# Performance work log

Hardware: AMD Instinct MI355X
Metric: run time of the kernel (lower is better)

Reference implementation:

```python
import jax, jax.numpy as jnp
import numpy as np

N, C_IN, C_OUT, H, W = 16, 256, 256, 32, 32
K = 9  # 3x3 kernel


def setup_inputs() -> dict:
    key = jax.random.key(0)
    k1, k2, k3 = jax.random.split(key, 3)
    x = jax.random.normal(k1, (N, C_IN, H, W), dtype=jnp.float32)
    # offsets as produced upstream from anchors: (N, H*W, 18)
    offset = jax.random.normal(k2, (N, H * W, 2 * K), dtype=jnp.float32)
    # DeformConv weight (no bias), kaiming-ish scale
    weight = jax.random.normal(k3, (C_OUT, C_IN, 3, 3), dtype=jnp.float32) * 0.02
    return {"x": x, "offset": offset, "weight": weight}


def _deform_conv3x3(x, offset_nchw, weight):
    """DeformConv v1, kernel 3x3, stride 1, padding 1, dilation 1,
    groups=1, deformable_groups=1, zero padding outside borders."""
    n, c, h, w = x.shape
    o = weight.shape[0]
    # offset channel layout: (dy_k, dx_k) pairs for k = 0..8
    off = offset_nchw.reshape(n, K, 2, h, w)
    dy = off[:, :, 0]  # (N,K,H,W)
    dx = off[:, :, 1]
    ky = (jnp.arange(K) // 3 - 1).astype(x.dtype)  # kernel row offsets -1,0,1
    kx = (jnp.arange(K) % 3 - 1).astype(x.dtype)
    base_y = jnp.arange(h, dtype=x.dtype)[None, None, :, None]
    base_x = jnp.arange(w, dtype=x.dtype)[None, None, None, :]
    py = base_y + ky[None, :, None, None] + dy  # (N,K,H,W) sample rows
    px = base_x + kx[None, :, None, None] + dx  # (N,K,H,W) sample cols

    y0 = jnp.floor(py)
    x0 = jnp.floor(px)
    ly = py - y0  # fractional parts
    lx = px - x0

    x_flat = x.reshape(n, c, h * w)

    def corner(yi, xi, wgt):
        valid = (yi >= 0) & (yi <= h - 1) & (xi >= 0) & (xi <= w - 1)
        yc = jnp.clip(yi, 0, h - 1).astype(jnp.int32)
        xc = jnp.clip(xi, 0, w - 1).astype(jnp.int32)
        idx = (yc * w + xc).reshape(n, K * h * w)
        g = jax.vmap(lambda xf, i: xf[:, i])(x_flat, idx)  # (N,C,K*H*W)
        wv = (wgt * valid.astype(x.dtype)).reshape(n, 1, K * h * w)
        return g * wv

    val = (corner(y0, x0, (1 - ly) * (1 - lx))
           + corner(y0, x0 + 1, (1 - ly) * lx)
           + corner(y0 + 1, x0, ly * (1 - lx))
           + corner(y0 + 1, x0 + 1, ly * lx))
    val = val.reshape(n, c, K, h, w)  # sampled im2col columns
    return jnp.einsum('nckhw,ock->nohw', val, weight.reshape(o, c, K))


def reference(x, offset, weight):
    n, _, h, w = x.shape
    assert h * w == offset.shape[1]
    # AdaptiveConv.forward: (N, HW, 18) -> (N, 18, H, W)
    offset_nchw = jnp.transpose(offset, (0, 2, 1)).reshape(n, 2 * K, h, w)
    return _deform_conv3x3(x, offset_nchw, weight)
```

## Files before the change

kernel.cpp:

```cpp
#include <hip/hip_runtime.h>

#define NB   16
#define CIN  256
#define COUT 256
#define HH   32
#define WW   32
#define HW   1024
#define KK   9
#define CK   2304

typedef __bf16 bf16x8 __attribute__((ext_vector_type(8)));
typedef float  f32x4  __attribute__((ext_vector_type(4)));

__device__ __forceinline__ unsigned short f2bf(float f) {
    unsigned int u = __float_as_uint(f);
    u += 0x7FFFu + ((u >> 16) & 1u);
    return (unsigned short)(u >> 16);
}
__device__ __forceinline__ float bfhi(unsigned int u) {
    return __uint_as_float(u & 0xFFFF0000u);
}
__device__ __forceinline__ float bflo(unsigned int u) {
    return __uint_as_float(u << 16);
}

typedef const __attribute__((address_space(1))) void* gas_ptr;
typedef __attribute__((address_space(3))) void* las_ptr;

__device__ __forceinline__ void async16(const void* g, void* l) {
    __builtin_amdgcn_global_load_lds((gas_ptr)g, (las_ptr)l, 16, 0, 0);
}

#define SB() __builtin_amdgcn_sched_barrier(0)
#define SYNC() do { SB(); asm volatile("s_waitcnt lgkmcnt(0)" ::: "memory"); SB(); \
                    __builtin_amdgcn_s_barrier(); SB(); } while (0)

__global__ __launch_bounds__(256) void wconv_kernel(const float* __restrict__ w,
                                                    unsigned short* __restrict__ wbf) {
    __shared__ float ls[CK];
    const int o = blockIdx.x;
    const float* wo = w + (size_t)o * CK;
#pragma unroll
    for (int i = threadIdx.x; i < CK; i += 256) ls[i] = wo[i];
    __syncthreads();
    unsigned short* dst = wbf + (size_t)o * CK;
#pragma unroll
    for (int i = threadIdx.x; i < CK; i += 256) {
        int k = i >> 8, c = i & 255;
        dst[i] = f2bf(ls[c * KK + k]);
    }
}

__global__ __launch_bounds__(256) void xt_kernel(const float* __restrict__ x,
                                                 unsigned short* __restrict__ xtb) {
    __shared__ float ls[64][65];
    const int c0  = blockIdx.x * 64;
    const int hw0 = blockIdx.y * 64;
    const int n   = blockIdx.z;
    const int t   = threadIdx.x;
    {
        int c = t >> 2, q = t & 3;
        const float4* base = (const float4*)(x + ((size_t)(n * CIN + c0 + c)) * HW + hw0 + q * 16);
#pragma unroll
        for (int j = 0; j < 4; ++j) {
            float4 v = base[j];
            ls[c][q * 16 + j * 4 + 0] = v.x;
            ls[c][q * 16 + j * 4 + 1] = v.y;
            ls[c][q * 16 + j * 4 + 2] = v.z;
            ls[c][q * 16 + j * 4 + 3] = v.w;
        }
    }
    __syncthreads();
    {
        int hw = t >> 2, seg = (t & 3) * 16;
        unsigned int dw[8];
#pragma unroll
        for (int j = 0; j < 8; ++j) {
            float f0 = ls[seg + 2 * j][hw];
            float f1 = ls[seg + 2 * j + 1][hw];
            dw[j] = (unsigned)f2bf(f0) | ((unsigned)f2bf(f1) << 16);
        }
        uint4* dst = (uint4*)(xtb + ((size_t)(n * HW + hw0 + hw)) * CIN + c0 + seg);
        dst[0] = *(uint4*)&dw[0];
        dst[1] = *(uint4*)&dw[4];
    }
}

__global__ __launch_bounds__(512, 2) void fused_kernel(const unsigned short* __restrict__ wbf,
                                                       const unsigned short* __restrict__ xtb,
                                                       const float* __restrict__ off,
                                                       float* __restrict__ out) {
    __shared__ unsigned short As[3][256 * 64];
    __shared__ unsigned short Bs[2][64 * 64];

    const int tid  = threadIdx.x;
    const int wv   = tid >> 6;
    const int lane = tid & 63;
    const int quad = lane >> 4;
    const int l15  = lane & 15;

    const int hw_local = tid >> 3;
    const int seg      = tid & 7;

    const int id  = blockIdx.x;
    const int n   = ((id & 7) << 1) | ((id >> 3) & 1);
    const int hw0 = (id >> 4) * 64;

    const int hw = hw0 + hw_local;
    const int h  = hw >> 5, w = hw & 31;

    const int srow   = lane >> 3;
    const int schunk = (lane & 7) ^ (srow & 7);

    const uint4*  xb4  = (const uint4*)(xtb + (size_t)n * HW * CIN);
    const float2* offp = (const float2*)(off + ((size_t)n * HW + hw) * (2 * KK));

    f32x4 acc[2][4] = {};

    auto setup2 = [&](float2 o, int tapv, float* wg, int* ix) {
        float py = (float)(h + tapv / 3 - 1) + o.x;
        float px = (float)(w + tapv % 3 - 1) + o.y;
        float y0f = floorf(py), x0f = floorf(px);
        float ly = py - y0f, lx = px - x0f;
        int y0 = (int)y0f, x0 = (int)x0f;
#pragma unroll
        for (int c2 = 0; c2 < 4; ++c2) {
            int yy = y0 + (c2 >> 1);
            int xx = x0 + (c2 & 1);
            float wy = (c2 >> 1) ? ly : 1.0f - ly;
            float wx = (c2 & 1) ? lx : 1.0f - lx;
            bool v = (yy >= 0) && (yy < HH) && (xx >= 0) && (xx < WW);
            wg[c2] = v ? wy * wx : 0.0f;
            int yc = yy < 0 ? 0 : (yy > HH - 1 ? HH - 1 : yy);
            int xc = xx < 0 ? 0 : (xx > WW - 1 ? WW - 1 : xx);
            ix[c2] = yc * WW + xc;
        }
    };

    auto loadc = [&](uint4 cr[4], const int* ix, int q) {
#pragma unroll
        for (int c2 = 0; c2 < 4; ++c2)
            cr[c2] = xb4[(size_t)ix[c2] * 32 + q * 8 + seg];
    };

    auto dmaA = [&](int ai, int kblk) {
        const unsigned short* wsrc = wbf + (size_t)kblk * 64 + (size_t)srow * CK + schunk * 8;
        unsigned short* dst = &As[ai][0];
#pragma unroll
        for (int j = 0; j < 4; ++j) {
            int rb = wv * 32 + j * 8;
            async16(wsrc + (size_t)rb * CK, dst + rb * 64);
        }
    };

    auto lerpB = [&](int bi, const uint4 cr[4], const float* wg) {
        unsigned u0[4], u1[4], u2[4], u3[4];
        *(uint4*)u0 = cr[0]; *(uint4*)u1 = cr[1];
        *(uint4*)u2 = cr[2]; *(uint4*)u3 = cr[3];
        unsigned dw[4];
#pragma unroll
        for (int d = 0; d < 4; ++d) {
            float lo = wg[0] * bflo(u0[d]) + wg[1] * bflo(u1[d])
                     + wg[2] * bflo(u2[d]) + wg[3] * bflo(u3[d]);
            float hi = wg[0] * bfhi(u0[d]) + wg[1] * bfhi(u1[d])
                     + wg[2] * bfhi(u2[d]) + wg[3] * bfhi(u3[d]);
            dw[d] = (unsigned)f2bf(lo) | ((unsigned)f2bf(hi) << 16);
        }
        *(uint4*)&Bs[bi][hw_local * 64 + (seg ^ (hw_local & 7)) * 8] = *(uint4*)dw;
    };

    auto mfma_step = [&](int ai, int bi) {
        const unsigned short* Ap = &As[ai][0];
        const unsigned short* Bp = &Bs[bi][0];
        bf16x8 af[2][2], bfr[4][2];
#pragma unroll
        for (int mi = 0; mi < 2; ++mi)
#pragma unroll
            for (int hh = 0; hh < 2; ++hh) {
                int row = wv * 32 + mi * 16 + l15;
                int ch  = (hh * 4 + quad) ^ (row & 7);
                af[mi][hh] = *(const bf16x8*)(Ap + row * 64 + ch * 8);
            }
#pragma unroll
        for (int ni = 0; ni < 4; ++ni)
#pragma unroll
            for (int hh = 0; hh < 2; ++hh) {
                int row = ni * 16 + l15;
                int ch  = (hh * 4 + quad) ^ (row & 7);
                bfr[ni][hh] = *(const bf16x8*)(Bp + row * 64 + ch * 8);
            }
        __builtin_amdgcn_s_setprio(1);
#pragma unroll
        for (int mi = 0; mi < 2; ++mi)
#pragma unroll
            for (int ni = 0; ni < 4; ++ni) {
                acc[mi][ni] = __builtin_amdgcn_mfma_f32_16x16x32_bf16(af[mi][0], bfr[ni][0], acc[mi][ni], 0, 0, 0);
                acc[mi][ni] = __builtin_amdgcn_mfma_f32_16x16x32_bf16(af[mi][1], bfr[ni][1], acc[mi][ni], 0, 0, 0);
            }
        __builtin_amdgcn_s_setprio(0);
    };

    float wgc[4], wgn[4];
    int   ixc[4], ixn[4];
    uint4 crA[4], crB[4];
    {
        float2 o0 = offp[0];
        setup2(o0, 0, wgc, ixc);
        dmaA(0, 0);
        dmaA(1, 1);
        SB();
        loadc(crA, ixc, 0);
        loadc(crB, ixc, 1);
        SB();
        lerpB(0, crA, wgc);
        SYNC();
    }

    int i0 = 0;
#pragma unroll 1
    for (int tap = 0; tap < 9; ++tap) {
        const int i1 = (i0 == 2) ? 0 : i0 + 1;
        const int i2 = (i1 == 2) ? 0 : i1 + 1;
        const int kb = tap * 4;
        const bool more = (tap < 8);

        dmaA(i2, kb + 2);
        SB();
        lerpB(1, crB, wgc);
        SB();
        loadc(crA, ixc, 2);
        SB();
        mfma_step(i0, 0);
        SYNC();

        dmaA(i0, kb + 3);
        SB();
        lerpB(0, crA, wgc);
        SB();
        loadc(crB, ixc, 3);
        SB();
        mfma_step(i1, 1);
        SYNC();

        float2 onx = {};
        if (more) onx = offp[tap + 1];
        SB();
        if (more) dmaA(i1, kb + 4);
        SB();
        lerpB(1, crB, wgc);
        SB();
        if (more) { setup2(onx, tap + 1, wgn, ixn); loadc(crA, ixn, 0); }
        SB();
        mfma_step(i2, 0);
        SYNC();

        if (more) {
            dmaA(i2, kb + 5);
            SB();
            lerpB(0, crA, wgn);
            SB();
            loadc(crB, ixn, 1);
#pragma unroll
            for (int c2 = 0; c2 < 4; ++c2) { wgc[c2] = wgn[c2]; ixc[c2] = ixn[c2]; }
            SB();
            mfma_step(i0, 1);
            SYNC();
        } else {
            mfma_step(i0, 1);
        }
        i0 = i1;
    }

    float* opnt = out + (size_t)n * COUT * HW + hw0;
#pragma unroll
    for (int mi = 0; mi < 2; ++mi)
#pragma unroll
        for (int ni = 0; ni < 4; ++ni) {
            int col = ni * 16 + l15;
#pragma unroll
            for (int rr = 0; rr < 4; ++rr) {
                int row = wv * 32 + mi * 16 + quad * 4 + rr;
                opnt[(size_t)row * HW + col] = acc[mi][ni][rr];
            }
        }
}

extern "C" void kernel_launch(void* const* d_in, const int* in_sizes, int n_in,
                              void* d_out, int out_size, void* d_ws, size_t ws_size,
                              hipStream_t stream) {
    const float* x   = (const float*)d_in[0];
    const float* off = (const float*)d_in[1];
    const float* wt  = (const float*)d_in[2];
    float* out = (float*)d_out;

    unsigned short* wbf = (unsigned short*)d_ws;
    unsigned short* xtb = (unsigned short*)((char*)d_ws + 1179648);

    wconv_kernel<<<256, 256, 0, stream>>>(wt, wbf);
    xt_kernel<<<dim3(4, 16, 16), 256, 0, stream>>>(x, xtb);
    fused_kernel<<<256, 512, 0, stream>>>(wbf, xtb, off, out);
}
```

Before: 122.1 us.

## Split output channels across two blocks and merge prep kernels into one launch

Each fused block now covers 128 output channels with 256 threads instead of 256 channels with 512 threads, doubling the grid to 512 blocks so more CUs are busy. Each thread now gathers and interpolates two 16-byte chunks per corner, and the A tile in LDS shrinks, which cuts LDS use per block. The weight conversion and x transpose kernels are merged into one launch to save launch overhead. The cost is that the deformable bilinear gather and interpolation for each B tile is now done twice, once per output half.

```diff
diff --git a/kernel.cpp b/kernel.cpp
--- a/kernel.cpp
+++ b/kernel.cpp
@@ -35,29 +35,33 @@
 #define SYNC() do { SB(); asm volatile("s_waitcnt lgkmcnt(0)" ::: "memory"); SB(); \
                     __builtin_amdgcn_s_barrier(); SB(); } while (0)
 
-__global__ __launch_bounds__(256) void wconv_kernel(const float* __restrict__ w,
-                                                    unsigned short* __restrict__ wbf) {
-    __shared__ float ls[CK];
-    const int o = blockIdx.x;
-    const float* wo = w + (size_t)o * CK;
-#pragma unroll
-    for (int i = threadIdx.x; i < CK; i += 256) ls[i] = wo[i];
-    __syncthreads();
-    unsigned short* dst = wbf + (size_t)o * CK;
-#pragma unroll
-    for (int i = threadIdx.x; i < CK; i += 256) {
-        int k = i >> 8, c = i & 255;
-        dst[i] = f2bf(ls[c * KK + k]);
-    }
-}
-
-__global__ __launch_bounds__(256) void xt_kernel(const float* __restrict__ x,
-                                                 unsigned short* __restrict__ xtb) {
-    __shared__ float ls[64][65];
-    const int c0  = blockIdx.x * 64;
-    const int hw0 = blockIdx.y * 64;
-    const int n   = blockIdx.z;
-    const int t   = threadIdx.x;
+__global__ __launch_bounds__(256) void prep_kernel(const float* __restrict__ w,
+                                                   unsigned short* __restrict__ wbf,
+                                                   const float* __restrict__ x,
+                                                   unsigned short* __restrict__ xtb) {
+    __shared__ float lsbuf[64 * 65];
+    const int t = threadIdx.x;
+
+    if (blockIdx.x < 256) {
+        const int o = blockIdx.x;
+        const float* wo = w + (size_t)o * CK;
+#pragma unroll
+        for (int i = t; i < CK; i += 256) lsbuf[i] = wo[i];
+        __syncthreads();
+        unsigned short* dst = wbf + (size_t)o * CK;
+#pragma unroll
+        for (int i = t; i < CK; i += 256) {
+            int k = i >> 8, c = i & 255;
+            dst[i] = f2bf(lsbuf[c * KK + k]);
+        }
+        return;
+    }
+
+    float (*ls)[65] = (float(*)[65])lsbuf;
+    const int id  = blockIdx.x - 256;
+    const int c0  = (id & 3) << 6;
+    const int hw0 = ((id >> 2) & 15) << 6;
+    const int n   = id >> 6;
     {
         int c = t >> 2, q = t & 3;
         const float4* base = (const float4*)(x + ((size_t)(n * CIN + c0 + c)) * HW + hw0 + q * 16);
@@ -86,11 +90,11 @@
     }
 }
 
-__global__ __launch_bounds__(512, 2) void fused_kernel(const unsigned short* __restrict__ wbf,
+__global__ __launch_bounds__(256, 2) void fused_kernel(const unsigned short* __restrict__ wbf,
                                                        const unsigned short* __restrict__ xtb,
                                                        const float* __restrict__ off,
                                                        float* __restrict__ out) {
-    __shared__ unsigned short As[3][256 * 64];
+    __shared__ unsigned short As[3][128 * 64];
     __shared__ unsigned short Bs[2][64 * 64];
 
     const int tid  = threadIdx.x;
@@ -99,12 +103,17 @@
     const int quad = lane >> 4;
     const int l15  = lane & 15;
 
-    const int hw_local = tid >> 3;
-    const int seg      = tid & 7;
-
-    const int id  = blockIdx.x;
-    const int n   = ((id & 7) << 1) | ((id >> 3) & 1);
-    const int hw0 = (id >> 4) * 64;
+    const int hw_local = tid >> 2;
+    const int seg4     = tid & 2 ? (tid & 3) : (tid & 3);
+    const int sg       = tid & 3;
+
+    const int id    = blockIdx.x;
+    const int xcd   = id & 7;
+    const int g     = id >> 3;
+    const int n     = (xcd << 1) | (g & 1);
+    const int tt    = g >> 1;
+    const int hw0   = (tt >> 1) << 6;
+    const int ohalf = tt & 1;
 
     const int hw = hw0 + hw_local;
     const int h  = hw >> 5, w = hw & 31;
@@ -114,6 +123,7 @@
 
     const uint4*  xb4  = (const uint4*)(xtb + (size_t)n * HW * CIN);
     const float2* offp = (const float2*)(off + ((size_t)n * HW + hw) * (2 * KK));
+    const unsigned short* wbase = wbf + (size_t)(ohalf * 128 + srow) * CK + schunk * 8;
 
     f32x4 acc[2][4] = {};
 
@@ -137,14 +147,17 @@
         }
     };
 
-    auto loadc = [&](uint4 cr[4], const int* ix, int q) {
-#pragma unroll
-        for (int c2 = 0; c2 < 4; ++c2)
-            cr[c2] = xb4[(size_t)ix[c2] * 32 + q * 8 + seg];
+    auto loadc = [&](uint4 cr[2][4], const int* ix, int q) {
+#pragma unroll
+        for (int c2 = 0; c2 < 4; ++c2) {
+            size_t base = (size_t)ix[c2] * 32 + q * 8 + sg * 2;
+            cr[0][c2] = xb4[base];
+            cr[1][c2] = xb4[base + 1];
+        }
     };
 
     auto dmaA = [&](int ai, int kblk) {
-        const unsigned short* wsrc = wbf + (size_t)kblk * 64 + (size_t)srow * CK + schunk * 8;
+        const unsigned short* wsrc = wbase + (size_t)kblk * 64;
         unsigned short* dst = &As[ai][0];
 #pragma unroll
         for (int j = 0; j < 4; ++j) {
@@ -153,20 +166,23 @@
         }
     };
 
-    auto lerpB = [&](int bi, const uint4 cr[4], const float* wg) {
-        unsigned u0[4], u1[4], u2[4], u3[4];
-        *(uint4*)u0 = cr[0]; *(uint4*)u1 = cr[1];
-        *(uint4*)u2 = cr[2]; *(uint4*)u3 = cr[3];
-        unsigned dw[4];
-#pragma unroll
-        for (int d = 0; d < 4; ++d) {
-            float lo = wg[0] * bflo(u0[d]) + wg[1] * bflo(u1[d])
-                     + wg[2] * bflo(u2[d]) + wg[3] * bflo(u3[d]);
-            float hi = wg[0] * bfhi(u0[d]) + wg[1] * bfhi(u1[d])
-                     + wg[2] * bfhi(u2[d]) + wg[3] * bfhi(u3[d]);
-            dw[d] = (unsigned)f2bf(lo) | ((unsigned)f2bf(hi) << 16);
-        }
-        *(uint4*)&Bs[bi][hw_local * 64 + (seg ^ (hw_local & 7)) * 8] = *(uint4*)dw;
+    auto lerpB = [&](int bi, const uint4 cr[2][4], const float* wg) {
+#pragma unroll
+        for (int hh = 0; hh < 2; ++hh) {
+            unsigned u0[4], u1[4], u2[4], u3[4];
+            *(uint4*)u0 = cr[hh][0]; *(uint4*)u1 = cr[hh][1];
+            *(uint4*)u2 = cr[hh][2]; *(uint4*)u3 = cr[hh][3];
+            unsigned dw[4];
+#pragma unroll
+            for (int d = 0; d < 4; ++d) {
+                float lo = wg[0] * bflo(u0[d]) + wg[1] * bflo(u1[d])
+                         + wg[2] * bflo(u2[d]) + wg[3] * bflo(u3[d]);
+                float hi = wg[0] * bfhi(u0[d]) + wg[1] * bfhi(u1[d])
+                         + wg[2] * bfhi(u2[d]) + wg[3] * bfhi(u3[d]);
+                dw[d] = (unsigned)f2bf(lo) | ((unsigned)f2bf(hi) << 16);
+            }
+            *(uint4*)&Bs[bi][hw_local * 64 + ((sg * 2 + hh) ^ (hw_local & 7)) * 8] = *(uint4*)dw;
+        }
     };
 
     auto mfma_step = [&](int ai, int bi) {
@@ -202,7 +218,7 @@
 
     float wgc[4], wgn[4];
     int   ixc[4], ixn[4];
-    uint4 crA[4], crB[4];
+    uint4 crA[2][4], crB[2][4];
     {
         float2 o0 = offp[0];
         setup2(o0, 0, wgc, ixc);
@@ -271,7 +287,7 @@
         i0 = i1;
     }
 
-    float* opnt = out + (size_t)n * COUT * HW + hw0;
+    float* opnt = out + (size_t)n * COUT * HW + (size_t)(ohalf * 128) * HW + hw0;
 #pragma unroll
     for (int mi = 0; mi < 2; ++mi)
 #pragma unroll
@@ -296,7 +312,6 @@
     unsigned short* wbf = (unsigned short*)d_ws;
     unsigned short* xtb = (unsigned short*)((char*)d_ws + 1179648);
 
-    wconv_kernel<<<256, 256, 0, stream>>>(wt, wbf);
-    xt_kernel<<<dim3(4, 16, 16), 256, 0, stream>>>(x, xtb);
-    fused_kernel<<<256, 512, 0, stream>>>(wbf, xtb, off, out);
-}
+    prep_kernel<<<1280, 256, 0, stream>>>(wt, wbf, x, xtb);
+    fused_kernel<<<512, 256, 0, stream>>>(wbf, xtb, off, out);
+}
```

Measured after the change: 125.7 us. 1.03x slower.

## Merge three kernels into one persistent kernel with a grid-wide barrier

Applied to the files above, without the earlier changes.

Folds the weight bf16 conversion and the x transpose/convert kernels into the main fused kernel. Each block first does its share of the preprocessing, then all blocks meet at a global atomic-counter barrier before the deform-conv GEMM. This is meant to remove two kernel launches and the gaps between them. In exchange it relies on all 256 blocks being resident at once to avoid deadlock, and it adds the cost of a grid-wide spin barrier.

```diff
diff --git a/kernel.cpp b/kernel.cpp
--- a/kernel.cpp
+++ b/kernel.cpp
@@ -35,65 +35,73 @@
 #define SYNC() do { SB(); asm volatile("s_waitcnt lgkmcnt(0)" ::: "memory"); SB(); \
                     __builtin_amdgcn_s_barrier(); SB(); } while (0)
 
-__global__ __launch_bounds__(256) void wconv_kernel(const float* __restrict__ w,
-                                                    unsigned short* __restrict__ wbf) {
-    __shared__ float ls[CK];
-    const int o = blockIdx.x;
-    const float* wo = w + (size_t)o * CK;
-#pragma unroll
-    for (int i = threadIdx.x; i < CK; i += 256) ls[i] = wo[i];
-    __syncthreads();
-    unsigned short* dst = wbf + (size_t)o * CK;
-#pragma unroll
-    for (int i = threadIdx.x; i < CK; i += 256) {
-        int k = i >> 8, c = i & 255;
-        dst[i] = f2bf(ls[c * KK + k]);
-    }
-}
-
-__global__ __launch_bounds__(256) void xt_kernel(const float* __restrict__ x,
-                                                 unsigned short* __restrict__ xtb) {
-    __shared__ float ls[64][65];
-    const int c0  = blockIdx.x * 64;
-    const int hw0 = blockIdx.y * 64;
-    const int n   = blockIdx.z;
-    const int t   = threadIdx.x;
-    {
-        int c = t >> 2, q = t & 3;
-        const float4* base = (const float4*)(x + ((size_t)(n * CIN + c0 + c)) * HW + hw0 + q * 16);
-#pragma unroll
-        for (int j = 0; j < 4; ++j) {
-            float4 v = base[j];
-            ls[c][q * 16 + j * 4 + 0] = v.x;
-            ls[c][q * 16 + j * 4 + 1] = v.y;
-            ls[c][q * 16 + j * 4 + 2] = v.z;
-            ls[c][q * 16 + j * 4 + 3] = v.w;
-        }
-    }
-    __syncthreads();
-    {
-        int hw = t >> 2, seg = (t & 3) * 16;
-        unsigned int dw[8];
-#pragma unroll
-        for (int j = 0; j < 8; ++j) {
-            float f0 = ls[seg + 2 * j][hw];
-            float f1 = ls[seg + 2 * j + 1][hw];
-            dw[j] = (unsigned)f2bf(f0) | ((unsigned)f2bf(f1) << 16);
-        }
-        uint4* dst = (uint4*)(xtb + ((size_t)(n * HW + hw0 + hw)) * CIN + c0 + seg);
-        dst[0] = *(uint4*)&dw[0];
-        dst[1] = *(uint4*)&dw[4];
-    }
-}
-
-__global__ __launch_bounds__(512, 2) void fused_kernel(const unsigned short* __restrict__ wbf,
-                                                       const unsigned short* __restrict__ xtb,
-                                                       const float* __restrict__ off,
-                                                       float* __restrict__ out) {
+__device__ unsigned g_ctr = 0;
+
+__global__ __launch_bounds__(512, 2) void mono_kernel(const float* __restrict__ wt,
+                                                      const float* __restrict__ x,
+                                                      const float* __restrict__ off,
+                                                      unsigned short* __restrict__ wbf,
+                                                      unsigned short* __restrict__ xtb,
+                                                      float* __restrict__ out) {
     __shared__ unsigned short As[3][256 * 64];
     __shared__ unsigned short Bs[2][64 * 64];
 
     const int tid  = threadIdx.x;
+    const int id   = blockIdx.x;
+
+    {
+        float* scratch = (float*)&As[0][0];
+
+        const float* wo = wt + (size_t)id * CK;
+        for (int i = tid; i < CK; i += 512) scratch[i] = wo[i];
+        __syncthreads();
+        unsigned short* wdst = wbf + (size_t)id * CK;
+        for (int i = tid; i < CK; i += 512) {
+            int k = i >> 8, c = i & 255;
+            wdst[i] = f2bf(scratch[c * KK + k]);
+        }
+        __syncthreads();
+
+        const int xcd  = id & 7, jb = id >> 3;
+        const int half = tid >> 8, t = tid & 255;
+        float* lt = scratch + half * (64 * 65);
+#pragma unroll 1
+        for (int it = 0; it < 2; ++it) {
+            int idx  = jb * 4 + it * 2 + half;
+            int n    = (xcd << 1) + (idx >> 6);
+            int rest = idx & 63;
+            int hw0  = (rest >> 2) << 6;
+            int c0   = (rest & 3) << 6;
+            {
+                int c = t >> 2, q = t & 3;
+                const float4* base = (const float4*)(x + ((size_t)(n * CIN + c0 + c)) * HW + hw0 + q * 16);
+#pragma unroll
+                for (int j2 = 0; j2 < 4; ++j2) {
+                    float4 v = base[j2];
+                    lt[c * 65 + q * 16 + j2 * 4 + 0] = v.x;
+                    lt[c * 65 + q * 16 + j2 * 4 + 1] = v.y;
+                    lt[c * 65 + q * 16 + j2 * 4 + 2] = v.z;
+                    lt[c * 65 + q * 16 + j2 * 4 + 3] = v.w;
+                }
+            }
+            __syncthreads();
+            {
+                int hwl = t >> 2, seg = (t & 3) * 16;
+                unsigned dw2[8];
+#pragma unroll
+                for (int j2 = 0; j2 < 8; ++j2) {
+                    float f0 = lt[(seg + 2 * j2) * 65 + hwl];
+                    float f1 = lt[(seg + 2 * j2 + 1) * 65 + hwl];
+                    dw2[j2] = (unsigned)f2bf(f0) | ((unsigned)f2bf(f1) << 16);
+                }
+                uint4* d2 = (uint4*)(xtb + ((size_t)(n * HW + hw0 + hwl)) * CIN + c0 + seg);
+                d2[0] = *(uint4*)&dw2[0];
+                d2[1] = *(uint4*)&dw2[4];
+            }
+            __syncthreads();
+        }
+    }
+
     const int wv   = tid >> 6;
     const int lane = tid & 63;
     const int quad = lane >> 4;
@@ -102,7 +110,6 @@
     const int hw_local = tid >> 3;
     const int seg      = tid & 7;
 
-    const int id  = blockIdx.x;
     const int n   = ((id & 7) << 1) | ((id >> 3) & 1);
     const int hw0 = (id >> 4) * 64;
 
@@ -114,6 +121,21 @@
 
     const uint4*  xb4  = (const uint4*)(xtb + (size_t)n * HW * CIN);
     const float2* offp = (const float2*)(off + ((size_t)n * HW + hw) * (2 * KK));
+
+    float2 o0 = offp[0];
+
+    __threadfence();
+    __syncthreads();
+    if (tid == 0) {
+        unsigned ticket = __hip_atomic_fetch_add(&g_ctr, 1u, __ATOMIC_ACQ_REL,
+                                                 __HIP_MEMORY_SCOPE_AGENT);
+        unsigned target = ((ticket >> 8) + 1) << 8;
+        while (__hip_atomic_load(&g_ctr, __ATOMIC_ACQUIRE,
+                                 __HIP_MEMORY_SCOPE_AGENT) < target)
+            __builtin_amdgcn_s_sleep(2);
+    }
+    __syncthreads();
+    __threadfence();
 
     f32x4 acc[2][4] = {};
 
@@ -204,7 +226,6 @@
     int   ixc[4], ixn[4];
     uint4 crA[4], crB[4];
     {
-        float2 o0 = offp[0];
         setup2(o0, 0, wgc, ixc);
         dmaA(0, 0);
         dmaA(1, 1);
@@ -296,7 +317,5 @@
     unsigned short* wbf = (unsigned short*)d_ws;
     unsigned short* xtb = (unsigned short*)((char*)d_ws + 1179648);
 
-    wconv_kernel<<<256, 256, 0, stream>>>(wt, wbf);
-    xt_kernel<<<dim3(4, 16, 16), 256, 0, stream>>>(x, xtb);
-    fused_kernel<<<256, 512, 0, stream>>>(wbf, xtb, off, out);
-}
+    mono_kernel<<<256, 512, 0, stream>>>(wt, x, off, wbf, xtb, out);
+}
```

Result: slower. 212.8 us (+74.3%).
